# Performance work log

Measured on AMD Instinct MI355X. Metric: run time of the kernel, lower is better.

## Reference

```python
import jax, jax.numpy as jnp
import numpy as np

N, B, D_IN, HID = 1024, 8, 256, 256
L, SH, LH, GH = 2, 2, 4, 2
H = SH + LH + GH
DH = HID // H
EPS = 1e-5


def _sinusoidal_pe(n, d):
    pos = np.arange(n, dtype=np.float32)[:, None]
    i = np.arange(d, dtype=np.float32)[None, :]
    angle = pos / np.power(10000.0, (2.0 * np.floor(i / 2.0)) / d)
    pe = np.where((np.arange(d) % 2) == 0, np.sin(angle), np.cos(angle))
    return jnp.asarray(pe, jnp.float32)  # (n, d)


def _ln(x, g, b):
    mu = x.mean(-1, keepdims=True)
    var = ((x - mu) ** 2).mean(-1, keepdims=True)
    return (x - mu) * jax.lax.rsqrt(var + EPS) * g + b


def setup_inputs() -> dict:
    key = jax.random.key(0)
    ks = jax.random.split(key, 16)
    s = 0.02
    inp = {
        "nodes": jax.random.normal(ks[0], (N, B, D_IN), jnp.float32),
        "dist": jax.random.randint(ks[1], (B, N, N), 0, 6, jnp.int32),
        "W_in": jax.random.normal(ks[2], (D_IN, HID), jnp.float32) * s,
        "b_in": jnp.zeros((HID,), jnp.float32),
        "ln_in_g": jnp.ones((HID,), jnp.float32),
        "ln_in_b": jnp.zeros((HID,), jnp.float32),
        "Wqkv": jax.random.normal(ks[3], (L, HID, 3 * HID), jnp.float32) * s,
        "bqkv": jnp.zeros((L, 3 * HID), jnp.float32),
        "Wo": jax.random.normal(ks[4], (L, HID, HID), jnp.float32) * s,
        "bo": jnp.zeros((L, HID), jnp.float32),
        "ln1_g": jnp.ones((L, HID), jnp.float32),
        "ln1_b": jnp.zeros((L, HID), jnp.float32),
        "W1": jax.random.normal(ks[5], (L, HID, 2 * HID), jnp.float32) * s,
        "b1": jnp.zeros((L, 2 * HID), jnp.float32),
        "W2": jax.random.normal(ks[6], (L, 2 * HID, HID), jnp.float32) * s,
        "b2": jnp.zeros((L, HID), jnp.float32),
        "ln2_g": jnp.ones((L, HID), jnp.float32),
        "ln2_b": jnp.zeros((L, HID), jnp.float32),
        "bn_g": jnp.ones((HID,), jnp.float32),
        "bn_b": jnp.zeros((HID,), jnp.float32),
    }
    return inp


def reference(nodes, dist, W_in, b_in, ln_in_g, ln_in_b, Wqkv, bqkv, Wo, bo,
              ln1_g, ln1_b, W1, b1, W2, b2, ln2_g, ln2_b, bn_g, bn_b):
    # positional embedding (sinusoidal, added) + dense + LayerNorm; dropout=eval (identity)
    x = nodes + _sinusoidal_pe(N, D_IN)[:, None, :]          # (N,B,D_IN)
    x = _ln(x @ W_in + b_in, ln_in_g, ln_in_b)               # (N,B,HID)

    # dist_to_mask: per-head-group allowed patterns; True in torch mask = disallowed
    short = (dist == 1)[:, None]                             # (B,1,N,N)
    longm = (dist >= 1)[:, None]
    allowed = jnp.concatenate([
        jnp.broadcast_to(short, (B, SH, N, N)),
        jnp.broadcast_to(longm, (B, LH, N, N)),
        jnp.ones((B, GH, N, N), bool),
    ], axis=1)                                               # (B,H,N,N)
    bias = jnp.where(allowed, 0.0, -jnp.inf).astype(x.dtype)

    scale = 1.0 / np.sqrt(DH)
    for l in range(L):
        qkv = x @ Wqkv[l] + bqkv[l]                          # (N,B,3*HID)
        q, k, v = jnp.split(qkv, 3, axis=-1)
        def heads(t):  # (N,B,HID) -> (B,H,N,DH)
            return t.reshape(N, B, H, DH).transpose(1, 2, 0, 3)
        q, k, v = heads(q), heads(k), heads(v)
        s = jnp.einsum('bhnd,bhmd->bhnm', q, k) * scale + bias
        a = jax.nn.softmax(s, axis=-1)
        o = jnp.einsum('bhnm,bhmd->bhnd', a, v)              # (B,H,N,DH)
        o = o.transpose(2, 0, 1, 3).reshape(N, B, HID)
        x = _ln(x + o @ Wo[l] + bo[l], ln1_g[l], ln1_b[l])   # post-norm
        f = jax.nn.relu(x @ W1[l] + b1[l]) @ W2[l] + b2[l]
        x = _ln(x + f, ln2_g[l], ln2_b[l])

    y = x[0]                                                 # (B,HID) first position
    mu = y.mean(0)
    var = ((y - mu) ** 2).mean(0)
    return (y - mu) * jax.lax.rsqrt(var + EPS) * bn_g + bn_b
```

## Files before the change

kernel.cpp:

```cpp
#include <hip/hip_runtime.h>
#include <math.h>

constexpr int Nn = 1024, Bb = 8, HIDc = 256, Hh = 8, DHc = 32;

typedef __bf16 bf16x8 __attribute__((ext_vector_type(8)));
typedef __bf16 bf16x4 __attribute__((ext_vector_type(4)));
typedef float  f32x4  __attribute__((ext_vector_type(4)));

struct WCvtArgs {
    const float* src[9];
    int K[9], M[9], dstOff[9], tiles[9];
};

__global__ __launch_bounds__(256)
void prep_k(WCvtArgs a, __bf16* __restrict__ Wt,
            const int* __restrict__ dist, unsigned char* __restrict__ mp,
            const float* __restrict__ nodes, __bf16* __restrict__ xinb)
{
    __shared__ float ts[32][33];
    const int tid = threadIdx.x;
    if (blockIdx.x < 1088) {
        int bid = blockIdx.x, i = 0;
        while (bid >= a.tiles[i]) { bid -= a.tiles[i]; ++i; }
        const int K = a.K[i], M = a.M[i];
        const int tilesM = M >> 5;
        const int m0 = (bid % tilesM) << 5, k0 = (bid / tilesM) << 5;
        const float* src = a.src[i];
        __bf16* dst = Wt + a.dstOff[i];
        const int tx = tid & 31, ty = tid >> 5;
        #pragma unroll
        for (int j = 0; j < 4; ++j)
            ts[ty + 8 * j][tx] = src[(size_t)(k0 + ty + 8 * j) * M + m0 + tx];
        __syncthreads();
        #pragma unroll
        for (int j = 0; j < 4; ++j)
            dst[(size_t)(m0 + ty + 8 * j) * K + k0 + tx] = (__bf16)ts[tx][ty + 8 * j];
    } else if (blockIdx.x < 3136) {
        const int idx = (blockIdx.x - 1088) * 256 + tid;
        const int quad = idx & 3, c = (idx >> 2) & 15, q = (idx >> 6) & 1023, b = idx >> 16;
        const int* dp = dist + ((((size_t)b << 10) + q) << 10) + c * 64 + quad * 4;
        uchar4 out;
        unsigned char* po = &out.x;
        #pragma unroll
        for (int t = 0; t < 4; ++t) {
            const int4 v = *(const int4*)(dp + t * 16);
            unsigned int code = 0;
            const int dd[4] = {v.x, v.y, v.z, v.w};
            #pragma unroll
            for (int r = 0; r < 4; ++r)
                code |= ((dd[r] == 1 ? 1u : 0u) | (dd[r] >= 1 ? 2u : 0u)) << (2 * r);
            po[t] = (unsigned char)code;
        }
        *(uchar4*)(mp + ((((size_t)b << 10) + q) << 8) + (c << 4) + (quad << 2)) = out;
    } else {
        const int idx = (blockIdx.x - 3136) * 256 + tid;
        const int token = idx >> 7, k2 = (idx & 127) * 2;
        const int b = token >> 10, n = token & 1023;
        const float e = (float)k2 * (1.0f / 256.0f);
        const float freq = exp2f(-13.287712379549449f * e);
        const float ang = (float)n * freq;
        const float2 nd = *(const float2*)(nodes + ((size_t)(n * 8 + b)) * 256 + k2);
        __bf16* p = xinb + (size_t)token * 256 + k2;
        p[0] = (__bf16)(nd.x + sinf(ang));
        p[1] = (__bf16)(nd.y + cosf(ang));
    }
}

template<int NCH>
__device__ __forceinline__ void gemm8(const bf16x8* af, const __bf16* __restrict__ wsrc,
                                      __bf16 (*wlds)[256][72], int mrow, int kcol,
                                      int ch, int col, int quad, f32x4* acc)
{
    constexpr int K = NCH * 64;
    bf16x8 wreg[8];
    #pragma unroll
    for (int i = 0; i < 8; ++i)
        wreg[i] = *(const bf16x8*)(wsrc + (size_t)(i * 32 + mrow) * K + kcol);
    __syncthreads();
    #pragma unroll
    for (int i = 0; i < 8; ++i)
        *(bf16x8*)&wlds[0][i * 32 + mrow][kcol] = wreg[i];
    if (NCH > 1) {
        #pragma unroll
        for (int i = 0; i < 8; ++i)
            wreg[i] = *(const bf16x8*)(wsrc + (size_t)(i * 32 + mrow) * K + 64 + kcol);
    }
    __syncthreads();
    #pragma unroll
    for (int t = 0; t < 8; ++t) acc[t] = (f32x4){0.f, 0.f, 0.f, 0.f};
    for (int ck = 0; ck < NCH; ++ck) {
        #pragma unroll
        for (int t = 0; t < 8; ++t)
            #pragma unroll
            for (int kc = 0; kc < 2; ++kc) {
                const bf16x8 bfr = *(const bf16x8*)(&wlds[ck & 1][ch * 128 + t * 16 + col][kc * 32 + quad * 8]);
                acc[t] = __builtin_amdgcn_mfma_f32_16x16x32_bf16(af[ck * 2 + kc], bfr, acc[t], 0, 0, 0);
            }
        if (ck + 1 < NCH) {
            #pragma unroll
            for (int i = 0; i < 8; ++i)
                *(bf16x8*)&wlds[(ck + 1) & 1][i * 32 + mrow][kcol] = wreg[i];
            if (ck + 2 < NCH) {
                #pragma unroll
                for (int i = 0; i < 8; ++i)
                    wreg[i] = *(const bf16x8*)(wsrc + (size_t)(i * 32 + mrow) * K + (ck + 2) * 64 + kcol);
            }
        }
        __syncthreads();
    }
}

template<bool RESID, bool FFN, bool QKV, bool N0ROWS, bool XGATE>
__global__ __launch_bounds__(256)
void layer_k(const __bf16* __restrict__ Ain, const float* __restrict__ xres,
             const __bf16* __restrict__ w0, const float* __restrict__ b0,
             const float* __restrict__ g1, const float* __restrict__ be1,
             const __bf16* __restrict__ w1, const float* __restrict__ b1_,
             const __bf16* __restrict__ w2, const float* __restrict__ b2_,
             const float* __restrict__ g2, const float* __restrict__ be2,
             const __bf16* __restrict__ wq, const float* __restrict__ bq, int qfull,
             float* __restrict__ xout,
             __bf16* __restrict__ qb, __bf16* __restrict__ kb, __bf16* __restrict__ vtb)
{
    __shared__ char smem[73728];
    __bf16 (*wlds)[256][72] = (__bf16 (*)[256][72])smem;
    __bf16 (*trans)[520] = (__bf16 (*)[520])smem;
    __shared__ float red[2][2][16][2];

    const int tid = threadIdx.x;
    const int lane = tid & 63;
    const int wv = tid >> 6;
    const int rt = wv >> 1, ch = wv & 1;
    const int col = lane & 15, quad = lane >> 4;
    const int row0 = blockIdx.x * 32;
    const int rowL = rt * 16 + col;
    const int mrow = tid >> 3, kcol = (tid & 7) * 8;
    const int trow = rt * 16 + quad * 4;

    const int rowAg = N0ROWS ? ((rowL & 7) << 10) : (row0 + rowL);

    bf16x8 afA[8];
    #pragma unroll
    for (int kc = 0; kc < 8; ++kc)
        afA[kc] = *(const bf16x8*)(Ain + (size_t)rowAg * 256 + kc * 32 + quad * 8);
    f32x4 acc[8];
    gemm8<4>(afA, w0, wlds, mrow, kcol, ch, col, quad, acc);

    float val[4][8];
    {
        float bb[8], gm[8], bt[8];
        #pragma unroll
        for (int t = 0; t < 8; ++t) {
            const int cc = ch * 128 + t * 16 + col;
            bb[t] = b0[cc]; gm[t] = g1[cc]; bt[t] = be1[cc];
        }
        #pragma unroll
        for (int r = 0; r < 4; ++r) {
            const int rg = N0ROWS ? (((trow + r) & 7) << 10) : (row0 + trow + r);
            float s1 = 0.f, s2 = 0.f;
            #pragma unroll
            for (int t = 0; t < 8; ++t) {
                float v = acc[t][r] + bb[t];
                if (RESID) v += xres[(size_t)rg * 256 + ch * 128 + t * 16 + col];
                val[r][t] = v; s1 += v; s2 += v * v;
            }
            s1 += __shfl_xor(s1, 1); s1 += __shfl_xor(s1, 2);
            s1 += __shfl_xor(s1, 4); s1 += __shfl_xor(s1, 8);
            s2 += __shfl_xor(s2, 1); s2 += __shfl_xor(s2, 2);
            s2 += __shfl_xor(s2, 4); s2 += __shfl_xor(s2, 8);
            if (col == 0) { red[rt][ch][quad * 4 + r][0] = s1; red[rt][ch][quad * 4 + r][1] = s2; }
        }
        __syncthreads();
        #pragma unroll
        for (int r = 0; r < 4; ++r) {
            const int qr = quad * 4 + r;
            const float s1 = red[rt][0][qr][0] + red[rt][1][qr][0];
            const float s2 = red[rt][0][qr][1] + red[rt][1][qr][1];
            const float mu = s1 * (1.0f / 256.0f);
            const float rv = rsqrtf(s2 * (1.0f / 256.0f) - mu * mu + 1e-5f);
            #pragma unroll
            for (int t = 0; t < 8; ++t) {
                const float o = (val[r][t] - mu) * rv * gm[t] + bt[t];
                val[r][t] = o;
                trans[trow + r][ch * 128 + t * 16 + col] = (__bf16)o;
                if (!FFN)
                    xout[(size_t)(row0 + trow + r) * 256 + ch * 128 + t * 16 + col] = o;
            }
        }
        __syncthreads();
    }

    if (FFN) {
        bf16x8 af1[8];
        #pragma unroll
        for (int kc = 0; kc < 8; ++kc)
            af1[kc] = *(const bf16x8*)(&trans[rowL][kc * 32 + quad * 8]);
        bf16x4 h1p[2][8];
        #pragma unroll
        for (int mh = 0; mh < 2; ++mh) {
            f32x4 accb[8];
            gemm8<4>(af1, w1 + (size_t)mh * 256 * 256, wlds, mrow, kcol, ch, col, quad, accb);
            #pragma unroll
            for (int t = 0; t < 8; ++t) {
                const float bbv = b1_[mh * 256 + ch * 128 + t * 16 + col];
                #pragma unroll
                for (int r = 0; r < 4; ++r)
                    h1p[mh][t][r] = (__bf16)fmaxf(accb[t][r] + bbv, 0.f);
            }
        }
        __syncthreads();
        #pragma unroll
        for (int mh = 0; mh < 2; ++mh)
            #pragma unroll
            for (int t = 0; t < 8; ++t)
                #pragma unroll
                for (int r = 0; r < 4; ++r)
                    trans[trow + r][mh * 256 + ch * 128 + t * 16 + col] = h1p[mh][t][r];
        __syncthreads();

        bf16x8 af2[16];
        #pragma unroll
        for (int kc = 0; kc < 16; ++kc)
            af2[kc] = *(const bf16x8*)(&trans[rowL][kc * 32 + quad * 8]);
        f32x4 accc[8];
        gemm8<8>(af2, w2, wlds, mrow, kcol, ch, col, quad, accc);

        float bb[8], gm[8], bt[8];
        #pragma unroll
        for (int t = 0; t < 8; ++t) {
            const int cc = ch * 128 + t * 16 + col;
            bb[t] = b2_[cc]; gm[t] = g2[cc]; bt[t] = be2[cc];
        }
        #pragma unroll
        for (int r = 0; r < 4; ++r) {
            float s1 = 0.f, s2 = 0.f;
            #pragma unroll
            for (int t = 0; t < 8; ++t) {
                const float v = accc[t][r] + bb[t] + val[r][t];
                val[r][t] = v; s1 += v; s2 += v * v;
            }
            s1 += __shfl_xor(s1, 1); s1 += __shfl_xor(s1, 2);
            s1 += __shfl_xor(s1, 4); s1 += __shfl_xor(s1, 8);
            s2 += __shfl_xor(s2, 1); s2 += __shfl_xor(s2, 2);
            s2 += __shfl_xor(s2, 4); s2 += __shfl_xor(s2, 8);
            if (col == 0) { red[rt][ch][quad * 4 + r][0] = s1; red[rt][ch][quad * 4 + r][1] = s2; }
        }
        __syncthreads();
        #pragma unroll
        for (int r = 0; r < 4; ++r) {
            const int qr = quad * 4 + r;
            const float s1 = red[rt][0][qr][0] + red[rt][1][qr][0];
            const float s2 = red[rt][0][qr][1] + red[rt][1][qr][1];
            const float mu = s1 * (1.0f / 256.0f);
            const float rv = rsqrtf(s2 * (1.0f / 256.0f) - mu * mu + 1e-5f);
            const int rl = trow + r;
            const int rg = N0ROWS ? ((rl & 7) << 10) : (row0 + rl);
            #pragma unroll
            for (int t = 0; t < 8; ++t) {
                const float o = (val[r][t] - mu) * rv * gm[t] + bt[t];
                if (QKV) trans[rl][ch * 128 + t * 16 + col] = (__bf16)o;
                bool wr;
                if (N0ROWS)      wr = (rl < 8);
                else if (XGATE)  wr = ((rg & 1023) == 0);
                else             wr = true;
                if (wr) xout[(size_t)rg * 256 + ch * 128 + t * 16 + col] = o;
            }
        }
        __syncthreads();
    }

    if (QKV) {
        bf16x8 af3[8];
        #pragma unroll
        for (int kc = 0; kc < 8; ++kc)
            af3[kc] = *(const bf16x8*)(&trans[rowL][kc * 32 + quad * 8]);
        const int bq_ = row0 >> 10;
        const int n0q = (row0 & 1023) + trow;
        const bool qneed = qfull || ((row0 & 1023) == 0);
        for (int cg = 0; cg < 3; ++cg) {
            if (cg == 0 && !qneed) continue;
            f32x4 accq[8];
            gemm8<4>(af3, wq + (size_t)cg * 256 * 256, wlds, mrow, kcol, ch, col, quad, accq);
            if (cg == 2) {
                #pragma unroll
                for (int t = 0; t < 8; ++t) {
                    const int cc = ch * 128 + t * 16 + col;
                    const int h = cc >> 5, dh = cc & 31;
                    const float bbv = bq[512 + cc];
                    bf16x4 p;
                    #pragma unroll
                    for (int r = 0; r < 4; ++r) p[r] = (__bf16)(accq[t][r] + bbv);
                    *(bf16x4*)(vtb + ((((size_t)(bq_ * 8 + h)) * 32 + dh) << 10) + n0q) = p;
                }
            } else {
                const float qs = (cg == 0) ? 0.25505402616305625f : 1.0f;
                __bf16* dst = (cg == 0) ? qb : kb;
                #pragma unroll
                for (int t = 0; t < 8; ++t) {
                    const int cc = ch * 128 + t * 16 + col;
                    const int h = cc >> 5, dh = cc & 31;
                    const float bbv = bq[cg * 256 + cc];
                    #pragma unroll
                    for (int r = 0; r < 4; ++r)
                        dst[((((size_t)(bq_ * 8 + h)) << 10) + n0q + r) * 32 + dh] =
                            (__bf16)((accq[t][r] + bbv) * qs);
                }
            }
        }
    }
}

__global__ __launch_bounds__(256)
void attn_mfma(const __bf16* __restrict__ Qb, const __bf16* __restrict__ Kb,
               const __bf16* __restrict__ Vt, const unsigned char* __restrict__ MP,
               __bf16* __restrict__ O)
{
    __shared__ __bf16 pbuf[2][4][2][16][72];
    const int tid = threadIdx.x;
    const int lane = tid & 63;
    const int wv = tid >> 6;
    const int col = lane & 15;
    const int quad = lane >> 4;
    const int xr = blockIdx.x;
    const int bh = ((xr & 7) << 3) | (xr >> 3);
    const int b = bh >> 3, h = bh & 7;
    const int qbase = blockIdx.y * 128 + wv * 32;
    const int hsel = (h < 2) ? 0 : 1;
    const bool masked = (h < 6);

    bf16x8 qf[2];
    #pragma unroll
    for (int j = 0; j < 2; ++j)
        qf[j] = *(const bf16x8*)(Qb + ((size_t)bh * Nn + qbase + j * 16 + col) * DHc + quad * 8);

    bf16x8 onesf;
    {
        const __bf16 one = (__bf16)1.0f, zero = (__bf16)0.0f;
        #pragma unroll
        for (int j = 0; j < 8; ++j) onesf[j] = (col == 0) ? one : zero;
    }

    f32x4 O0[2], O1[2], OL[2];
    #pragma unroll
    for (int j = 0; j < 2; ++j) {
        O0[j] = (f32x4){0.f, 0.f, 0.f, 0.f};
        O1[j] = (f32x4){0.f, 0.f, 0.f, 0.f};
        OL[j] = (f32x4){0.f, 0.f, 0.f, 0.f};
    }
    const f32x4 zf = {0.f, 0.f, 0.f, 0.f};
    const __bf16* kbase = Kb + (size_t)bh * Nn * DHc;

    bf16x8 kf[4];
    #pragma unroll
    for (int t = 0; t < 4; ++t)
        kf[t] = *(const bf16x8*)(kbase + (size_t)(t * 16 + col) * DHc + quad * 8);

    for (int c = 0; c < 16; ++c) {
        bf16x8 kn[4];
        if (c < 15)
            #pragma unroll
            for (int t = 0; t < 4; ++t)
                kn[t] = *(const bf16x8*)(kbase + (size_t)((c + 1) * 64 + t * 16 + col) * DHc + quad * 8);
        uchar4 mk[2];
        if (masked)
            #pragma unroll
            for (int j = 0; j < 2; ++j)
                mk[j] = *(const uchar4*)(MP + ((((size_t)b << 10) + qbase + j * 16 + col) << 8)
                                            + (c << 4) + (quad << 2));
        #pragma unroll
        for (int j = 0; j < 2; ++j) {
            f32x4 S[4];
            #pragma unroll
            for (int t = 0; t < 4; ++t)
                S[t] = __builtin_amdgcn_mfma_f32_16x16x32_bf16(kf[t], qf[j], zf, 0, 0, 0);
            if (masked) {
                const unsigned char mb[4] = {mk[j].x, mk[j].y, mk[j].z, mk[j].w};
                #pragma unroll
                for (int t = 0; t < 4; ++t)
                    #pragma unroll
                    for (int r = 0; r < 4; ++r)
                        if (!((mb[t] >> (2 * r + hsel)) & 1)) S[t][r] = -INFINITY;
            }
            #pragma unroll
            for (int t = 0; t < 4; ++t) {
                bf16x4 p4;
                #pragma unroll
                for (int r = 0; r < 4; ++r)
                    p4[r] = (__bf16)__builtin_amdgcn_exp2f(S[t][r]);
                *(bf16x4*)(&pbuf[c & 1][wv][j][col][t * 16 + quad * 4]) = p4;
            }
        }
        const __bf16* vp = Vt + (size_t)bh * DHc * Nn + c * 64 + quad * 8;
        #pragma unroll
        for (int kh = 0; kh < 2; ++kh) {
            const bf16x8 v0 = *(const bf16x8*)(vp + (size_t)col * Nn + kh * 32);
            const bf16x8 v1 = *(const bf16x8*)(vp + (size_t)(col + 16) * Nn + kh * 32);
            #pragma unroll
            for (int j = 0; j < 2; ++j) {
                const bf16x8 pf = *(const bf16x8*)(&pbuf[c & 1][wv][j][col][kh * 32 + quad * 8]);
                O0[j] = __builtin_amdgcn_mfma_f32_16x16x32_bf16(pf, v0, O0[j], 0, 0, 0);
                O1[j] = __builtin_amdgcn_mfma_f32_16x16x32_bf16(pf, v1, O1[j], 0, 0, 0);
                OL[j] = __builtin_amdgcn_mfma_f32_16x16x32_bf16(pf, onesf, OL[j], 0, 0, 0);
            }
        }
        if (c < 15)
            #pragma unroll
            for (int t = 0; t < 4; ++t) kf[t] = kn[t];
    }
    #pragma unroll
    for (int j = 0; j < 2; ++j)
        #pragma unroll
        for (int r = 0; r < 4; ++r) {
            const float Lr = __shfl(OL[j][r], lane & 48);
            const float inv = 1.0f / Lr;
            const int q = qbase + j * 16 + quad * 4 + r;
            __bf16* op = O + ((size_t)(b * 1024 + q)) * 256 + h * 32 + col;
            op[0]  = (__bf16)(O0[j][r] * inv);
            op[16] = (__bf16)(O1[j][r] * inv);
        }
}

__global__ __launch_bounds__(256)
void final_bn(const float* __restrict__ x, const float* __restrict__ g,
              const float* __restrict__ bta, float* __restrict__ out)
{
    const int d = threadIdx.x;
    float y[8]; float mu = 0.0f;
    #pragma unroll
    for (int i = 0; i < 8; ++i) { y[i] = x[((size_t)i << 18) + d]; mu += y[i]; }
    mu *= 0.125f;
    float var = 0.0f;
    #pragma unroll
    for (int i = 0; i < 8; ++i) { const float dd = y[i] - mu; var += dd * dd; }
    var *= 0.125f;
    const float r = rsqrtf(var + 1e-5f);
    const float gg = g[d], bb = bta[d];
    #pragma unroll
    for (int i = 0; i < 8; ++i) out[i * 256 + d] = (y[i] - mu) * r * gg + bb;
}

extern "C" void kernel_launch(void* const* d_in, const int* in_sizes, int n_in,
                              void* d_out, int out_size, void* d_ws, size_t ws_size,
                              hipStream_t stream)
{
    const float* nodes   = (const float*)d_in[0];
    const int*   dist    = (const int*)  d_in[1];
    const float* W_in    = (const float*)d_in[2];
    const float* b_in    = (const float*)d_in[3];
    const float* ln_in_g = (const float*)d_in[4];
    const float* ln_in_b = (const float*)d_in[5];
    const float* Wqkv    = (const float*)d_in[6];
    const float* bqkv    = (const float*)d_in[7];
    const float* Wo      = (const float*)d_in[8];
    const float* bo      = (const float*)d_in[9];
    const float* ln1_g   = (const float*)d_in[10];
    const float* ln1_b   = (const float*)d_in[11];
    const float* W1      = (const float*)d_in[12];
    const float* b1      = (const float*)d_in[13];
    const float* W2      = (const float*)d_in[14];
    const float* b2      = (const float*)d_in[15];
    const float* ln2_g   = (const float*)d_in[16];
    const float* ln2_b   = (const float*)d_in[17];
    const float* bn_g    = (const float*)d_in[18];
    const float* bn_b    = (const float*)d_in[19];

    char* ws = (char*)d_ws;
    float*  x   = (float*)(ws);
    unsigned char* mp = (unsigned char*)(ws + 8388608);
    __bf16* wt  = (__bf16*)(ws + 10485760);
    __bf16* qb  = (__bf16*)(ws + 12845056);
    __bf16* kb  = (__bf16*)(ws + 17039360);
    __bf16* vtb = (__bf16*)(ws + 21233664);
    __bf16* ob  = (__bf16*)(ws + 25427968);
    __bf16* xinb = ob;

    WCvtArgs wa;
    wa.src[0] = W_in;           wa.K[0] = 256; wa.M[0] = 256; wa.dstOff[0] = 0;
    wa.src[1] = Wqkv;           wa.K[1] = 256; wa.M[1] = 768; wa.dstOff[1] = 65536;
    wa.src[2] = Wqkv + 196608;  wa.K[2] = 256; wa.M[2] = 768; wa.dstOff[2] = 262144;
    wa.src[3] = Wo;             wa.K[3] = 256; wa.M[3] = 256; wa.dstOff[3] = 458752;
    wa.src[4] = Wo + 65536;     wa.K[4] = 256; wa.M[4] = 256; wa.dstOff[4] = 524288;
    wa.src[5] = W1;             wa.K[5] = 256; wa.M[5] = 512; wa.dstOff[5] = 589824;
    wa.src[6] = W1 + 131072;    wa.K[6] = 256; wa.M[6] = 512; wa.dstOff[6] = 720896;
    wa.src[7] = W2;             wa.K[7] = 512; wa.M[7] = 256; wa.dstOff[7] = 851968;
    wa.src[8] = W2 + 131072;    wa.K[8] = 512; wa.M[8] = 256; wa.dstOff[8] = 983040;
    for (int i = 0; i < 9; ++i) wa.tiles[i] = (wa.K[i] >> 5) * (wa.M[i] >> 5);

    prep_k<<<7232, 256, 0, stream>>>(wa, wt, dist, mp, nodes, xinb);

    layer_k<false, false, true, false, false><<<256, 256, 0, stream>>>(
        xinb, nullptr, wt, b_in, ln_in_g, ln_in_b,
        nullptr, nullptr, nullptr, nullptr, nullptr, nullptr,
        wt + 65536, bqkv, 1, x, qb, kb, vtb);

    attn_mfma<<<dim3(64, 8), 256, 0, stream>>>(qb, kb, vtb, mp, ob);

    layer_k<true, true, true, false, true><<<256, 256, 0, stream>>>(
        ob, x, wt + 458752, bo, ln1_g, ln1_b,
        wt + 589824, b1, wt + 851968, b2, ln2_g, ln2_b,
        wt + 262144, bqkv + 768, 0, x, qb, kb, vtb);

    attn_mfma<<<dim3(64, 1), 256, 0, stream>>>(qb, kb, vtb, mp, ob);

    layer_k<true, true, false, true, true><<<1, 256, 0, stream>>>(
        ob, x, wt + 524288, bo + 256, ln1_g + 256, ln1_b + 256,
        wt + 720896, b1 + 512, wt + 983040, b2 + 256, ln2_g + 256, ln2_b + 256,
        nullptr, nullptr, 0, x, nullptr, nullptr, nullptr);

    final_bn<<<1, 256, 0, stream>>>(x, bn_g, bn_b, (float*)d_out);
}
```

Baseline: 252.7 us.

## Halve layer kernel row tile to double grid, fuse final batchnorm

The fused layer kernel now handles 16 rows per block instead of 32, with each of the four waves computing a 64-column quarter. That doubles the grid from 256 to 512 blocks so more compute units are busy. The final BatchNorm is folded into the last single-block layer kernel via a BNOUT template flag, which removes one launch. In exchange, each block still loads the full weight matrices, so total weight traffic to LDS per output row doubles.

Measured after the change: 254.2 us. Within noise of the previous version (+0.6%).

```diff
diff --git a/kernel.cpp b/kernel.cpp
--- a/kernel.cpp
+++ b/kernel.cpp
@@ -67,9 +67,9 @@
 }
 
 template<int NCH>
-__device__ __forceinline__ void gemm8(const bf16x8* af, const __bf16* __restrict__ wsrc,
+__device__ __forceinline__ void gemm4(const bf16x8* af, const __bf16* __restrict__ wsrc,
                                       __bf16 (*wlds)[256][72], int mrow, int kcol,
-                                      int ch, int col, int quad, f32x4* acc)
+                                      int cq, int col, int quad, f32x4* acc)
 {
     constexpr int K = NCH * 64;
     bf16x8 wreg[8];
@@ -87,13 +87,13 @@
     }
     __syncthreads();
     #pragma unroll
-    for (int t = 0; t < 8; ++t) acc[t] = (f32x4){0.f, 0.f, 0.f, 0.f};
+    for (int t = 0; t < 4; ++t) acc[t] = (f32x4){0.f, 0.f, 0.f, 0.f};
     for (int ck = 0; ck < NCH; ++ck) {
         #pragma unroll
-        for (int t = 0; t < 8; ++t)
+        for (int t = 0; t < 4; ++t)
             #pragma unroll
             for (int kc = 0; kc < 2; ++kc) {
-                const bf16x8 bfr = *(const bf16x8*)(&wlds[ck & 1][ch * 128 + t * 16 + col][kc * 32 + quad * 8]);
+                const bf16x8 bfr = *(const bf16x8*)(&wlds[ck & 1][cq * 64 + t * 16 + col][kc * 32 + quad * 8]);
                 acc[t] = __builtin_amdgcn_mfma_f32_16x16x32_bf16(af[ck * 2 + kc], bfr, acc[t], 0, 0, 0);
             }
         if (ck + 1 < NCH) {
@@ -110,7 +110,7 @@
     }
 }
 
-template<bool RESID, bool FFN, bool QKV, bool N0ROWS, bool XGATE>
+template<bool RESID, bool FFN, bool QKV, bool N0ROWS, bool XGATE, bool BNOUT>
 __global__ __launch_bounds__(256)
 void layer_k(const __bf16* __restrict__ Ain, const float* __restrict__ xres,
              const __bf16* __restrict__ w0, const float* __restrict__ b0,
@@ -119,72 +119,72 @@
              const __bf16* __restrict__ w2, const float* __restrict__ b2_,
              const float* __restrict__ g2, const float* __restrict__ be2,
              const __bf16* __restrict__ wq, const float* __restrict__ bq, int qfull,
+             const float* __restrict__ bng, const float* __restrict__ bnb,
              float* __restrict__ xout,
              __bf16* __restrict__ qb, __bf16* __restrict__ kb, __bf16* __restrict__ vtb)
 {
     __shared__ char smem[73728];
     __bf16 (*wlds)[256][72] = (__bf16 (*)[256][72])smem;
     __bf16 (*trans)[520] = (__bf16 (*)[520])smem;
-    __shared__ float red[2][2][16][2];
+    __shared__ float red[4][16][2];
 
     const int tid = threadIdx.x;
     const int lane = tid & 63;
-    const int wv = tid >> 6;
-    const int rt = wv >> 1, ch = wv & 1;
+    const int cq = tid >> 6;
     const int col = lane & 15, quad = lane >> 4;
-    const int row0 = blockIdx.x * 32;
-    const int rowL = rt * 16 + col;
+    const int row0 = blockIdx.x * 16;
+    const int rowL = col;
     const int mrow = tid >> 3, kcol = (tid & 7) * 8;
-    const int trow = rt * 16 + quad * 4;
-
-    const int rowAg = N0ROWS ? ((rowL & 7) << 10) : (row0 + rowL);
+
+    const int rowAg = N0ROWS ? ((col & 7) << 10) : (row0 + col);
 
     bf16x8 afA[8];
     #pragma unroll
     for (int kc = 0; kc < 8; ++kc)
         afA[kc] = *(const bf16x8*)(Ain + (size_t)rowAg * 256 + kc * 32 + quad * 8);
-    f32x4 acc[8];
-    gemm8<4>(afA, w0, wlds, mrow, kcol, ch, col, quad, acc);
-
-    float val[4][8];
+    f32x4 acc[4];
+    gemm4<4>(afA, w0, wlds, mrow, kcol, cq, col, quad, acc);
+
+    float val[4][4];
     {
-        float bb[8], gm[8], bt[8];
-        #pragma unroll
-        for (int t = 0; t < 8; ++t) {
-            const int cc = ch * 128 + t * 16 + col;
+        float bb[4], gm[4], bt[4];
+        #pragma unroll
+        for (int t = 0; t < 4; ++t) {
+            const int cc = cq * 64 + t * 16 + col;
             bb[t] = b0[cc]; gm[t] = g1[cc]; bt[t] = be1[cc];
         }
         #pragma unroll
         for (int r = 0; r < 4; ++r) {
-            const int rg = N0ROWS ? (((trow + r) & 7) << 10) : (row0 + trow + r);
+            const int rl = quad * 4 + r;
+            const int rg = N0ROWS ? ((rl & 7) << 10) : (row0 + rl);
             float s1 = 0.f, s2 = 0.f;
             #pragma unroll
-            for (int t = 0; t < 8; ++t) {
+            for (int t = 0; t < 4; ++t) {
                 float v = acc[t][r] + bb[t];
-                if (RESID) v += xres[(size_t)rg * 256 + ch * 128 + t * 16 + col];
+                if (RESID) v += xres[(size_t)rg * 256 + cq * 64 + t * 16 + col];
                 val[r][t] = v; s1 += v; s2 += v * v;
             }
             s1 += __shfl_xor(s1, 1); s1 += __shfl_xor(s1, 2);
             s1 += __shfl_xor(s1, 4); s1 += __shfl_xor(s1, 8);
             s2 += __shfl_xor(s2, 1); s2 += __shfl_xor(s2, 2);
             s2 += __shfl_xor(s2, 4); s2 += __shfl_xor(s2, 8);
-            if (col == 0) { red[rt][ch][quad * 4 + r][0] = s1; red[rt][ch][quad * 4 + r][1] = s2; }
+            if (col == 0) { red[cq][rl][0] = s1; red[cq][rl][1] = s2; }
         }
         __syncthreads();
         #pragma unroll
         for (int r = 0; r < 4; ++r) {
-            const int qr = quad * 4 + r;
-            const float s1 = red[rt][0][qr][0] + red[rt][1][qr][0];
-            const float s2 = red[rt][0][qr][1] + red[rt][1][qr][1];
+            const int rl = quad * 4 + r;
+            const float s1 = red[0][rl][0] + red[1][rl][0] + red[2][rl][0] + red[3][rl][0];
+            const float s2 = red[0][rl][1] + red[1][rl][1] + red[2][rl][1] + red[3][rl][1];
             const float mu = s1 * (1.0f / 256.0f);
             const float rv = rsqrtf(s2 * (1.0f / 256.0f) - mu * mu + 1e-5f);
             #pragma unroll
-            for (int t = 0; t < 8; ++t) {
+            for (int t = 0; t < 4; ++t) {
                 const float o = (val[r][t] - mu) * rv * gm[t] + bt[t];
                 val[r][t] = o;
-                trans[trow + r][ch * 128 + t * 16 + col] = (__bf16)o;
+                trans[rl][cq * 64 + t * 16 + col] = (__bf16)o;
                 if (!FFN)
-                    xout[(size_t)(row0 + trow + r) * 256 + ch * 128 + t * 16 + col] = o;
+                    xout[(size_t)(row0 + rl) * 256 + cq * 64 + t * 16 + col] = o;
             }
         }
         __syncthreads();
@@ -195,14 +195,14 @@
         #pragma unroll
         for (int kc = 0; kc < 8; ++kc)
             af1[kc] = *(const bf16x8*)(&trans[rowL][kc * 32 + quad * 8]);
-        bf16x4 h1p[2][8];
+        bf16x4 h1p[2][4];
         #pragma unroll
         for (int mh = 0; mh < 2; ++mh) {
-            f32x4 accb[8];
-            gemm8<4>(af1, w1 + (size_t)mh * 256 * 256, wlds, mrow, kcol, ch, col, quad, accb);
-            #pragma unroll
-            for (int t = 0; t < 8; ++t) {
-                const float bbv = b1_[mh * 256 + ch * 128 + t * 16 + col];
+            f32x4 accb[4];
+            gemm4<4>(af1, w1 + (size_t)mh * 256 * 256, wlds, mrow, kcol, cq, col, quad, accb);
+            #pragma unroll
+            for (int t = 0; t < 4; ++t) {
+                const float bbv = b1_[mh * 256 + cq * 64 + t * 16 + col];
                 #pragma unroll
                 for (int r = 0; r < 4; ++r)
                     h1p[mh][t][r] = (__bf16)fmaxf(accb[t][r] + bbv, 0.f);
@@ -212,30 +212,31 @@
         #pragma unroll
         for (int mh = 0; mh < 2; ++mh)
             #pragma unroll
-            for (int t = 0; t < 8; ++t)
+            for (int t = 0; t < 4; ++t)
                 #pragma unroll
                 for (int r = 0; r < 4; ++r)
-                    trans[trow + r][mh * 256 + ch * 128 + t * 16 + col] = h1p[mh][t][r];
+                    trans[quad * 4 + r][mh * 256 + cq * 64 + t * 16 + col] = h1p[mh][t][r];
         __syncthreads();
 
         bf16x8 af2[16];
         #pragma unroll
         for (int kc = 0; kc < 16; ++kc)
             af2[kc] = *(const bf16x8*)(&trans[rowL][kc * 32 + quad * 8]);
-        f32x4 accc[8];
-        gemm8<8>(af2, w2, wlds, mrow, kcol, ch, col, quad, accc);
-
-        float bb[8], gm[8], bt[8];
-        #pragma unroll
-        for (int t = 0; t < 8; ++t) {
-            const int cc = ch * 128 + t * 16 + col;
+        f32x4 accc[4];
+        gemm4<8>(af2, w2, wlds, mrow, kcol, cq, col, quad, accc);
+
+        float bb[4], gm[4], bt[4];
+        #pragma unroll
+        for (int t = 0; t < 4; ++t) {
+            const int cc = cq * 64 + t * 16 + col;
             bb[t] = b2_[cc]; gm[t] = g2[cc]; bt[t] = be2[cc];
         }
         #pragma unroll
         for (int r = 0; r < 4; ++r) {
+            const int rl = quad * 4 + r;
             float s1 = 0.f, s2 = 0.f;
             #pragma unroll
-            for (int t = 0; t < 8; ++t) {
+            for (int t = 0; t < 4; ++t) {
                 const float v = accc[t][r] + bb[t] + val[r][t];
                 val[r][t] = v; s1 += v; s2 += v * v;
             }
@@ -243,27 +244,45 @@
             s1 += __shfl_xor(s1, 4); s1 += __shfl_xor(s1, 8);
             s2 += __shfl_xor(s2, 1); s2 += __shfl_xor(s2, 2);
             s2 += __shfl_xor(s2, 4); s2 += __shfl_xor(s2, 8);
-            if (col == 0) { red[rt][ch][quad * 4 + r][0] = s1; red[rt][ch][quad * 4 + r][1] = s2; }
+            if (col == 0) { red[cq][rl][0] = s1; red[cq][rl][1] = s2; }
         }
         __syncthreads();
         #pragma unroll
         for (int r = 0; r < 4; ++r) {
-            const int qr = quad * 4 + r;
-            const float s1 = red[rt][0][qr][0] + red[rt][1][qr][0];
-            const float s2 = red[rt][0][qr][1] + red[rt][1][qr][1];
+            const int rl = quad * 4 + r;
+            const float s1 = red[0][rl][0] + red[1][rl][0] + red[2][rl][0] + red[3][rl][0];
+            const float s2 = red[0][rl][1] + red[1][rl][1] + red[2][rl][1] + red[3][rl][1];
             const float mu = s1 * (1.0f / 256.0f);
             const float rv = rsqrtf(s2 * (1.0f / 256.0f) - mu * mu + 1e-5f);
-            const int rl = trow + r;
             const int rg = N0ROWS ? ((rl & 7) << 10) : (row0 + rl);
             #pragma unroll
-            for (int t = 0; t < 8; ++t) {
+            for (int t = 0; t < 4; ++t) {
                 const float o = (val[r][t] - mu) * rv * gm[t] + bt[t];
-                if (QKV) trans[rl][ch * 128 + t * 16 + col] = (__bf16)o;
-                bool wr;
-                if (N0ROWS)      wr = (rl < 8);
-                else if (XGATE)  wr = ((rg & 1023) == 0);
-                else             wr = true;
-                if (wr) xout[(size_t)rg * 256 + ch * 128 + t * 16 + col] = o;
+                val[r][t] = o;
+                if (QKV) trans[rl][cq * 64 + t * 16 + col] = (__bf16)o;
+                if (!BNOUT) {
+                    const bool wr = XGATE ? ((rg & 1023) == 0) : true;
+                    if (wr) xout[(size_t)rg * 256 + cq * 64 + t * 16 + col] = o;
+                }
+            }
+        }
+        if (BNOUT) {
+            #pragma unroll
+            for (int t = 0; t < 4; ++t) {
+                const int cc = cq * 64 + t * 16 + col;
+                float s1 = val[0][t] + val[1][t] + val[2][t] + val[3][t];
+                float s2 = val[0][t] * val[0][t] + val[1][t] * val[1][t]
+                         + val[2][t] * val[2][t] + val[3][t] * val[3][t];
+                s1 += __shfl_xor(s1, 16);
+                s2 += __shfl_xor(s2, 16);
+                const float mu = s1 * 0.125f;
+                const float rv = rsqrtf(s2 * 0.125f - mu * mu + 1e-5f);
+                const float gg = bng[cc], bb2 = bnb[cc];
+                if (quad < 2) {
+                    #pragma unroll
+                    for (int r = 0; r < 4; ++r)
+                        xout[(size_t)(quad * 4 + r) * 256 + cc] = (val[r][t] - mu) * rv * gg + bb2;
+                }
             }
         }
         __syncthreads();
@@ -275,16 +294,16 @@
         for (int kc = 0; kc < 8; ++kc)
             af3[kc] = *(const bf16x8*)(&trans[rowL][kc * 32 + quad * 8]);
         const int bq_ = row0 >> 10;
-        const int n0q = (row0 & 1023) + trow;
-        const bool qneed = qfull || ((row0 & 1023) == 0);
+        const int n0q = (row0 & 1023) + quad * 4;
+        const bool qneed = qfull || ((row0 & 1023) < 128);
         for (int cg = 0; cg < 3; ++cg) {
             if (cg == 0 && !qneed) continue;
-            f32x4 accq[8];
-            gemm8<4>(af3, wq + (size_t)cg * 256 * 256, wlds, mrow, kcol, ch, col, quad, accq);
+            f32x4 accq[4];
+            gemm4<4>(af3, wq + (size_t)cg * 256 * 256, wlds, mrow, kcol, cq, col, quad, accq);
             if (cg == 2) {
                 #pragma unroll
-                for (int t = 0; t < 8; ++t) {
-                    const int cc = ch * 128 + t * 16 + col;
+                for (int t = 0; t < 4; ++t) {
+                    const int cc = cq * 64 + t * 16 + col;
                     const int h = cc >> 5, dh = cc & 31;
                     const float bbv = bq[512 + cc];
                     bf16x4 p;
@@ -296,8 +315,8 @@
                 const float qs = (cg == 0) ? 0.25505402616305625f : 1.0f;
                 __bf16* dst = (cg == 0) ? qb : kb;
                 #pragma unroll
-                for (int t = 0; t < 8; ++t) {
-                    const int cc = ch * 128 + t * 16 + col;
+                for (int t = 0; t < 4; ++t) {
+                    const int cc = cq * 64 + t * 16 + col;
                     const int h = cc >> 5, dh = cc & 31;
                     const float bbv = bq[cg * 256 + cc];
                     #pragma unroll
@@ -418,25 +437,6 @@
             op[0]  = (__bf16)(O0[j][r] * inv);
             op[16] = (__bf16)(O1[j][r] * inv);
         }
-}
-
-__global__ __launch_bounds__(256)
-void final_bn(const float* __restrict__ x, const float* __restrict__ g,
-              const float* __restrict__ bta, float* __restrict__ out)
-{
-    const int d = threadIdx.x;
-    float y[8]; float mu = 0.0f;
-    #pragma unroll
-    for (int i = 0; i < 8; ++i) { y[i] = x[((size_t)i << 18) + d]; mu += y[i]; }
-    mu *= 0.125f;
-    float var = 0.0f;
-    #pragma unroll
-    for (int i = 0; i < 8; ++i) { const float dd = y[i] - mu; var += dd * dd; }
-    var *= 0.125f;
-    const float r = rsqrtf(var + 1e-5f);
-    const float gg = g[d], bb = bta[d];
-    #pragma unroll
-    for (int i = 0; i < 8; ++i) out[i * 256 + d] = (y[i] - mu) * r * gg + bb;
 }
 
 extern "C" void kernel_launch(void* const* d_in, const int* in_sizes, int n_in,
@@ -488,24 +488,22 @@
 
     prep_k<<<7232, 256, 0, stream>>>(wa, wt, dist, mp, nodes, xinb);
 
-    layer_k<false, false, true, false, false><<<256, 256, 0, stream>>>(
+    layer_k<false, false, true, false, false, false><<<512, 256, 0, stream>>>(
         xinb, nullptr, wt, b_in, ln_in_g, ln_in_b,
         nullptr, nullptr, nullptr, nullptr, nullptr, nullptr,
-        wt + 65536, bqkv, 1, x, qb, kb, vtb);
+        wt + 65536, bqkv, 1, nullptr, nullptr, x, qb, kb, vtb);
 
     attn_mfma<<<dim3(64, 8), 256, 0, stream>>>(qb, kb, vtb, mp, ob);
 
-    layer_k<true, true, true, false, true><<<256, 256, 0, stream>>>(
+    layer_k<true, true, true, false, true, false><<<512, 256, 0, stream>>>(
         ob, x, wt + 458752, bo, ln1_g, ln1_b,
         wt + 589824, b1, wt + 851968, b2, ln2_g, ln2_b,
-        wt + 262144, bqkv + 768, 0, x, qb, kb, vtb);
+        wt + 262144, bqkv + 768, 0, nullptr, nullptr, x, qb, kb, vtb);
 
     attn_mfma<<<dim3(64, 1), 256, 0, stream>>>(qb, kb, vtb, mp, ob);
 
-    layer_k<true, true, false, true, true><<<1, 256, 0, stream>>>(
+    layer_k<true, true, false, true, true, true><<<1, 256, 0, stream>>>(
         ob, x, wt + 524288, bo + 256, ln1_g + 256, ln1_b + 256,
         wt + 720896, b1 + 512, wt + 983040, b2 + 256, ln2_g + 256, ln2_b + 256,
-        nullptr, nullptr, 0, x, nullptr, nullptr, nullptr);
-
-    final_bn<<<1, 256, 0, stream>>>(x, bn_g, bn_b, (float*)d_out);
+        nullptr, nullptr, 0, bn_g, bn_b, (float*)d_out, nullptr, nullptr, nullptr);
 }
```
